# Kernel tuning notes

Measured on AMD Instinct MI355X. Metric: run time of the kernel, lower is better.

## Reference

```python
import jax, jax.numpy as jnp
import numpy as np

N = 16384   # must equal C**2 so the rel-pos embed broadcasts with x
C = 128     # in_channels
K = 9       # k (min legal for C=128: (2k-1)^2 >= 2C-1)
C_OUT = 256


def setup_inputs() -> dict:
    key = jax.random.key(0)
    k1, k2, k3 = jax.random.split(key, 3)
    x = jax.random.normal(k1, (N, C), dtype=jnp.float32)
    rel_pos_table = jax.random.normal(k2, ((2 * K - 1) ** 2, C), dtype=jnp.float32) * 0.02
    W = jax.random.normal(k3, (2 * C, C_OUT), dtype=jnp.float32) / np.float32(np.sqrt(2 * C))
    b = jnp.zeros((C_OUT,), dtype=jnp.float32)
    return {"x": x, "rel_pos_table": rel_pos_table, "W": W, "b": b}


def _knn_indices(x, k):
    # brute-force kNN (torch_cluster knn_graph, loop=False), dilation=1 -> no edge subsampling
    sq = jnp.sum(x * x, axis=-1)                       # [N]
    d = sq[:, None] + sq[None, :] - 2.0 * (x @ x.T)    # [N, N] squared distances
    d = d.at[jnp.diag_indices(x.shape[0])].set(jnp.inf)  # exclude self-loops
    _, idx = jax.lax.top_k(-d, k)                      # [N, k] nearest neighbors
    return idx


def reference(x, rel_pos_table, W, b):
    n, c = x.shape
    # 1) graph built on RAW x (before rel-pos add), as in the torch forward
    nbr = _knn_indices(x, K)                           # [N, K]
    # 2) learnable relative positional embedding: grid_size = x.shape[1] = C
    ar = jnp.arange(c)
    rel = (ar[:, None] - ar[None, :] + c - 1).reshape(-1)  # [C*C] == [N]
    x = x + rel_pos_table[rel]                         # [N, C]
    # 3) MRConv: max-relative aggregation + concat + 1x1 linear
    x_j = x[nbr]                                       # [N, K, C] neighbor gather
    m = jnp.max(x_j - x[:, None, :], axis=1)           # [N, C] max over neighbors
    return jnp.concatenate([x, m], axis=-1) @ W + b    # [N, C_OUT]
```

## Files before the change

kernel.cpp:

```cpp
#include <hip/hip_runtime.h>

#define NPTS 16384
#define CH 128
#define KNN 9
#define NCAND 12
#define NHALF 4
#define COUT 256
#define RG 8
#define RCAND 6

typedef __attribute__((ext_vector_type(8))) short bf16x8;
typedef __attribute__((ext_vector_type(4))) float f32x4;


__device__ __forceinline__ unsigned bfhi2(float x0, float x1) {
    unsigned u0 = __float_as_uint(x0), u1 = __float_as_uint(x1);
    unsigned r0 = (u0 + 0x7fffu + ((u0 >> 16) & 1u));
    unsigned r1 = (u1 + 0x7fffu + ((u1 >> 16) & 1u));
    return (r0 >> 16) | (r1 & 0xffff0000u);
}

struct TopL {
    float l0,l1,l2,l3,l4,l5,l6,l7,l8,l9,la,lb;
    int   m0,m1,m2,m3,m4,m5,m6,m7,m8,m9,ma,mb;
};
struct Top9 {
    float l0,l1,l2,l3,l4,l5,l6,l7,l8;
    int   m0,m1,m2,m3,m4,m5,m6,m7,m8;
};

__device__ __forceinline__ bool lexlt(float d, int g, float L, int M) {
    return d < L || (d == L && g < M);
}

__device__ __forceinline__ void ins12(TopL& T, float d, int g) {
    if (!lexlt(d, g, T.lb, T.mb)) return;
    bool b0 = lexlt(d,g,T.l0,T.m0);
    bool b1 = lexlt(d,g,T.l1,T.m1);
    bool b2 = lexlt(d,g,T.l2,T.m2);
    bool b3 = lexlt(d,g,T.l3,T.m3);
    bool b4 = lexlt(d,g,T.l4,T.m4);
    bool b5 = lexlt(d,g,T.l5,T.m5);
    bool b6 = lexlt(d,g,T.l6,T.m6);
    bool b7 = lexlt(d,g,T.l7,T.m7);
    bool b8 = lexlt(d,g,T.l8,T.m8);
    bool b9 = lexlt(d,g,T.l9,T.m9);
    bool ba = lexlt(d,g,T.la,T.ma);
    T.lb = ba ? T.la : d;               T.mb = ba ? T.ma : g;
    T.la = b9 ? T.l9 : (ba ? d : T.la); T.ma = b9 ? T.m9 : (ba ? g : T.ma);
    T.l9 = b8 ? T.l8 : (b9 ? d : T.l9); T.m9 = b8 ? T.m8 : (b9 ? g : T.m9);
    T.l8 = b7 ? T.l7 : (b8 ? d : T.l8); T.m8 = b7 ? T.m7 : (b8 ? g : T.m8);
    T.l7 = b6 ? T.l6 : (b7 ? d : T.l7); T.m7 = b6 ? T.m6 : (b7 ? g : T.m7);
    T.l6 = b5 ? T.l5 : (b6 ? d : T.l6); T.m6 = b5 ? T.m5 : (b6 ? g : T.m6);
    T.l5 = b4 ? T.l4 : (b5 ? d : T.l5); T.m5 = b4 ? T.m4 : (b5 ? g : T.m5);
    T.l4 = b3 ? T.l3 : (b4 ? d : T.l4); T.m4 = b3 ? T.m3 : (b4 ? g : T.m4);
    T.l3 = b2 ? T.l2 : (b3 ? d : T.l3); T.m3 = b2 ? T.m2 : (b3 ? g : T.m3);
    T.l2 = b1 ? T.l1 : (b2 ? d : T.l2); T.m2 = b1 ? T.m1 : (b2 ? g : T.m2);
    T.l1 = b0 ? T.l0 : (b1 ? d : T.l1); T.m1 = b0 ? T.m0 : (b1 ? g : T.m1);
    T.l0 = b0 ? d : T.l0;               T.m0 = b0 ? g : T.m0;
}

__device__ __forceinline__ void ins9(Top9& T, float d, int g) {
    if (!lexlt(d, g, T.l8, T.m8)) return;
    bool b0 = lexlt(d,g,T.l0,T.m0);
    bool b1 = lexlt(d,g,T.l1,T.m1);
    bool b2 = lexlt(d,g,T.l2,T.m2);
    bool b3 = lexlt(d,g,T.l3,T.m3);
    bool b4 = lexlt(d,g,T.l4,T.m4);
    bool b5 = lexlt(d,g,T.l5,T.m5);
    bool b6 = lexlt(d,g,T.l6,T.m6);
    bool b7 = lexlt(d,g,T.l7,T.m7);
    T.l8 = b7 ? T.l7 : d;               T.m8 = b7 ? T.m7 : g;
    T.l7 = b6 ? T.l6 : (b7 ? d : T.l7); T.m7 = b6 ? T.m6 : (b7 ? g : T.m7);
    T.l6 = b5 ? T.l5 : (b6 ? d : T.l6); T.m6 = b5 ? T.m5 : (b6 ? g : T.m6);
    T.l5 = b4 ? T.l4 : (b5 ? d : T.l5); T.m5 = b4 ? T.m4 : (b5 ? g : T.m5);
    T.l4 = b3 ? T.l3 : (b4 ? d : T.l4); T.m4 = b3 ? T.m3 : (b4 ? g : T.m4);
    T.l3 = b2 ? T.l2 : (b3 ? d : T.l3); T.m3 = b2 ? T.m2 : (b3 ? g : T.m3);
    T.l2 = b1 ? T.l1 : (b2 ? d : T.l2); T.m2 = b1 ? T.m1 : (b2 ? g : T.m2);
    T.l1 = b0 ? T.l0 : (b1 ? d : T.l1); T.m1 = b0 ? T.m0 : (b1 ? g : T.m1);
    T.l0 = b0 ? d : T.l0;               T.m0 = b0 ? g : T.m0;
}

__device__ __forceinline__ void merge_shfl(TopL& T, int mask) {
    TopL o;
    o.l0=__shfl_xor(T.l0,mask); o.m0=__shfl_xor(T.m0,mask);
    o.l1=__shfl_xor(T.l1,mask); o.m1=__shfl_xor(T.m1,mask);
    o.l2=__shfl_xor(T.l2,mask); o.m2=__shfl_xor(T.m2,mask);
    o.l3=__shfl_xor(T.l3,mask); o.m3=__shfl_xor(T.m3,mask);
    o.l4=__shfl_xor(T.l4,mask); o.m4=__shfl_xor(T.m4,mask);
    o.l5=__shfl_xor(T.l5,mask); o.m5=__shfl_xor(T.m5,mask);
    o.l6=__shfl_xor(T.l6,mask); o.m6=__shfl_xor(T.m6,mask);
    o.l7=__shfl_xor(T.l7,mask); o.m7=__shfl_xor(T.m7,mask);
    o.l8=__shfl_xor(T.l8,mask); o.m8=__shfl_xor(T.m8,mask);
    o.l9=__shfl_xor(T.l9,mask); o.m9=__shfl_xor(T.m9,mask);
    o.la=__shfl_xor(T.la,mask); o.ma=__shfl_xor(T.ma,mask);
    o.lb=__shfl_xor(T.lb,mask); o.mb=__shfl_xor(T.mb,mask);
    ins12(T,o.l0,o.m0); ins12(T,o.l1,o.m1); ins12(T,o.l2,o.m2);
    ins12(T,o.l3,o.m3); ins12(T,o.l4,o.m4); ins12(T,o.l5,o.m5);
    ins12(T,o.l6,o.m6); ins12(T,o.l7,o.m7); ins12(T,o.l8,o.m8);
    ins12(T,o.l9,o.m9); ins12(T,o.la,o.ma); ins12(T,o.lb,o.mb);
}

__device__ __forceinline__ void merge_shfl9(Top9& T, int mask) {
    Top9 o;
    o.l0=__shfl_xor(T.l0,mask); o.m0=__shfl_xor(T.m0,mask);
    o.l1=__shfl_xor(T.l1,mask); o.m1=__shfl_xor(T.m1,mask);
    o.l2=__shfl_xor(T.l2,mask); o.m2=__shfl_xor(T.m2,mask);
    o.l3=__shfl_xor(T.l3,mask); o.m3=__shfl_xor(T.m3,mask);
    o.l4=__shfl_xor(T.l4,mask); o.m4=__shfl_xor(T.m4,mask);
    o.l5=__shfl_xor(T.l5,mask); o.m5=__shfl_xor(T.m5,mask);
    o.l6=__shfl_xor(T.l6,mask); o.m6=__shfl_xor(T.m6,mask);
    o.l7=__shfl_xor(T.l7,mask); o.m7=__shfl_xor(T.m7,mask);
    o.l8=__shfl_xor(T.l8,mask); o.m8=__shfl_xor(T.m8,mask);
    ins9(T,o.l0,o.m0); ins9(T,o.l1,o.m1); ins9(T,o.l2,o.m2);
    ins9(T,o.l3,o.m3); ins9(T,o.l4,o.m4); ins9(T,o.l5,o.m5);
    ins9(T,o.l6,o.m6); ins9(T,o.l7,o.m7); ins9(T,o.l8,o.m8);
}

__global__ __launch_bounds__(256) void sqnp_kernel(const float* __restrict__ x,
                                                   float* __restrict__ sq) {
    const int i = blockIdx.x * 256 + threadIdx.x;
    const float4* row4 = (const float4*)(x + (size_t)i * CH);
    float r[8];
    {
        float4 a = row4[0], b = row4[1];
        r[0] = __fmul_rn(a.x, a.x); r[1] = __fmul_rn(a.y, a.y);
        r[2] = __fmul_rn(a.z, a.z); r[3] = __fmul_rn(a.w, a.w);
        r[4] = __fmul_rn(b.x, b.x); r[5] = __fmul_rn(b.y, b.y);
        r[6] = __fmul_rn(b.z, b.z); r[7] = __fmul_rn(b.w, b.w);
    }
#pragma unroll
    for (int g = 1; g < 16; ++g) {
        float4 a = row4[2 * g], b = row4[2 * g + 1];
        r[0] = __fadd_rn(r[0], __fmul_rn(a.x, a.x));
        r[1] = __fadd_rn(r[1], __fmul_rn(a.y, a.y));
        r[2] = __fadd_rn(r[2], __fmul_rn(a.z, a.z));
        r[3] = __fadd_rn(r[3], __fmul_rn(a.w, a.w));
        r[4] = __fadd_rn(r[4], __fmul_rn(b.x, b.x));
        r[5] = __fadd_rn(r[5], __fmul_rn(b.y, b.y));
        r[6] = __fadd_rn(r[6], __fmul_rn(b.z, b.z));
        r[7] = __fadd_rn(r[7], __fmul_rn(b.w, b.w));
    }
    float t0 = __fadd_rn(__fadd_rn(r[0], r[1]), __fadd_rn(r[2], r[3]));
    float t1 = __fadd_rn(__fadd_rn(r[4], r[5]), __fadd_rn(r[6], r[7]));
    sq[i] = __fadd_rn(t0, t1);
}

__global__ __launch_bounds__(256) void split_kernel(const float* __restrict__ x,
                                                    short* __restrict__ xhi) {
    const int P = blockIdx.x * 256 + threadIdx.x;
    const int r = P >> 4;
    const int s = P & 15;
    const int phys = s ^ (r & 15);
    const float4* src = (const float4*)(x + (size_t)r * CH) + s * 2;
    float4 f0 = src[0], f1 = src[1];
    uint4 h;
    h.x = bfhi2(f0.x, f0.y);
    h.y = bfhi2(f0.z, f0.w);
    h.z = bfhi2(f1.x, f1.y);
    h.w = bfhi2(f1.z, f1.w);
    *(uint4*)&xhi[(size_t)r * 128 + phys * 8] = h;
}

__global__ __launch_bounds__(256, 4) void knn_kernel(const short* __restrict__ xhi,
                                                     const float* __restrict__ sq,
                                                     unsigned short* __restrict__ cand) {
    __shared__ short Bhi[64 * 128];
    __shared__ float Dist[64 * 64];
    const int t = threadIdx.x;
    const int row0 = blockIdx.x * 64;
    const int half = blockIdx.y;
    const int ctbeg = half * (NPTS / NHALF);
    const int ctend = ctbeg + NPTS / NHALF;

    const int lane = t & 63;
    const int w = t >> 6;
    const int m = lane & 15;
    const int quad = lane >> 4;

#pragma unroll
    for (int it = 0; it < 4; ++it) {
        const int P = t + it * 256;
        *(uint4*)&Bhi[P * 8] = *(const uint4*)&xhi[(size_t)ctbeg * 128 + P * 8];
    }
    const short* arow = xhi + (size_t)(row0 + 16 * w + m) * 128;
    const bf16x8 a0 = *(const bf16x8*)&arow[((0 * 4 + quad) ^ m) * 8];
    const bf16x8 a1 = *(const bf16x8*)&arow[((1 * 4 + quad) ^ m) * 8];
    const bf16x8 a2 = *(const bf16x8*)&arow[((2 * 4 + quad) ^ m) * 8];
    const bf16x8 a3 = *(const bf16x8*)&arow[((3 * 4 + quad) ^ m) * 8];

    const float4 sqr4 = *(const float4*)&sq[row0 + 16 * w + quad * 4];

    TopL T;
    T.l0=T.l1=T.l2=T.l3=T.l4=T.l5=T.l6=T.l7=T.l8=T.l9=T.la=T.lb = __builtin_inff();
    T.m0=T.m1=T.m2=T.m3=T.m4=T.m5=T.m6=T.m7=T.m8=T.m9=T.ma=T.mb = 0x7fffffff;

    const int srow = t >> 2;
    const int sq4 = t & 3;
    const int srowg = row0 + srow;
    const float* drow = &Dist[srow * 64];
    const int sxor = srow & 63;

    for (int ct = ctbeg; ct < ctend; ct += 64) {
        __syncthreads();

        const float sqc0 = sq[ct + 0  + m];
        const float sqc1 = sq[ct + 16 + m];
        const float sqc2 = sq[ct + 32 + m];
        const float sqc3 = sq[ct + 48 + m];

        f32x4 acc0 = {0.f,0.f,0.f,0.f};
        f32x4 acc1 = {0.f,0.f,0.f,0.f};
        f32x4 acc2 = {0.f,0.f,0.f,0.f};
        f32x4 acc3 = {0.f,0.f,0.f,0.f};

#pragma unroll
        for (int kc = 0; kc < 4; ++kc) {
            const int ks = ((kc * 4 + quad) ^ m) * 8;
            const bf16x8 ah = (kc == 0) ? a0 : (kc == 1) ? a1 : (kc == 2) ? a2 : a3;
            bf16x8 bh0 = *(const bf16x8*)&Bhi[(0  + m) * 128 + ks];
            bf16x8 bh1 = *(const bf16x8*)&Bhi[(16 + m) * 128 + ks];
            bf16x8 bh2 = *(const bf16x8*)&Bhi[(32 + m) * 128 + ks];
            bf16x8 bh3 = *(const bf16x8*)&Bhi[(48 + m) * 128 + ks];
            acc0 = __builtin_amdgcn_mfma_f32_16x16x32_bf16(ah, bh0, acc0, 0, 0, 0);
            acc1 = __builtin_amdgcn_mfma_f32_16x16x32_bf16(ah, bh1, acc1, 0, 0, 0);
            acc2 = __builtin_amdgcn_mfma_f32_16x16x32_bf16(ah, bh2, acc2, 0, 0, 0);
            acc3 = __builtin_amdgcn_mfma_f32_16x16x32_bf16(ah, bh3, acc3, 0, 0, 0);
        }

#pragma unroll
        for (int reg = 0; reg < 4; ++reg) {
            const int row = 16 * w + quad * 4 + reg;
            const float sqr_r = (reg == 0) ? sqr4.x : (reg == 1) ? sqr4.y
                              : (reg == 2) ? sqr4.z : sqr4.w;
            const int c0 = 0  + m;
            const int c1 = 16 + m;
            const int c2 = 32 + m;
            const int c3 = 48 + m;
            Dist[row * 64 + (c0 ^ row)] = sqr_r + sqc0 - 2.f * acc0[reg];
            Dist[row * 64 + (c1 ^ row)] = sqr_r + sqc1 - 2.f * acc1[reg];
            Dist[row * 64 + (c2 ^ row)] = sqr_r + sqc2 - 2.f * acc2[reg];
            Dist[row * 64 + (c3 ^ row)] = sqr_r + sqc3 - 2.f * acc3[reg];
        }
        __syncthreads();

        const int ctn = ct + 64;
        uint4 pb0, pb1, pb2, pb3;
        if (ctn < ctend) {
            pb0 = *(const uint4*)&xhi[(size_t)ctn * 128 + (t +   0) * 8];
            pb1 = *(const uint4*)&xhi[(size_t)ctn * 128 + (t + 256) * 8];
            pb2 = *(const uint4*)&xhi[(size_t)ctn * 128 + (t + 512) * 8];
            pb3 = *(const uint4*)&xhi[(size_t)ctn * 128 + (t + 768) * 8];
        }

        float qd0 = __builtin_inff(), qd1 = __builtin_inff();
        int   qg0 = 0x7fffffff,      qg1 = 0x7fffffff;
        int   qn = 0;
#pragma unroll
        for (int k = 0; k < 16; ++k) {
            const int col = sq4 * 16 + k;
            const float d = drow[col ^ sxor];
            const int cg = ct + col;
            const bool pass = (cg != srowg) && lexlt(d, cg, T.lb, T.mb);
            if (pass) {
                if (qn >= 2) {
                    ins12(T, d, cg);
                } else if (qn == 0) {
                    qd0 = d; qg0 = cg;
                } else {
                    qd1 = d; qg1 = cg;
                }
                ++qn;
            }
        }
        if (qn > 0) ins12(T, qd0, qg0);
        if (qn > 1) ins12(T, qd1, qg1);

        if (ctn < ctend) {
            *(uint4*)&Bhi[(t +   0) * 8] = pb0;
            *(uint4*)&Bhi[(t + 256) * 8] = pb1;
            *(uint4*)&Bhi[(t + 512) * 8] = pb2;
            *(uint4*)&Bhi[(t + 768) * 8] = pb3;
        }
    }

    merge_shfl(T, 1);
    merge_shfl(T, 2);

    if (sq4 == 0) {
        unsigned short* cp_out = cand + (size_t)srowg * (NHALF * NCAND) + half * NCAND;
        cp_out[0]=(unsigned short)T.m0; cp_out[1]=(unsigned short)T.m1;
        cp_out[2]=(unsigned short)T.m2; cp_out[3]=(unsigned short)T.m3;
        cp_out[4]=(unsigned short)T.m4; cp_out[5]=(unsigned short)T.m5;
        cp_out[6]=(unsigned short)T.m6; cp_out[7]=(unsigned short)T.m7;
        cp_out[8]=(unsigned short)T.m8; cp_out[9]=(unsigned short)T.m9;
        cp_out[10]=(unsigned short)T.ma; cp_out[11]=(unsigned short)T.mb;
    }
}

__global__ __launch_bounds__(256) void refine_np_kernel(const float* __restrict__ x,
                                                        const float* __restrict__ sq,
                                                        const unsigned short* __restrict__ cand,
                                                        unsigned short* __restrict__ nbr) {
    const int gt = blockIdx.x * 256 + threadIdx.x;
    const int i = gt >> 3;
    const int g = gt & (RG - 1);
    const float4* X4 = (const float4*)x;
    const float sqi = sq[i];

    int ci[RCAND];
#pragma unroll
    for (int m = 0; m < RCAND; ++m)
        ci[m] = (int)cand[i * (NHALF * NCAND) + g * RCAND + m];
    float dot[RCAND];
#pragma unroll
    for (int m = 0; m < RCAND; ++m) dot[m] = 0.f;
#pragma unroll 4
    for (int c4 = 0; c4 < 32; ++c4) {
        float4 xv = X4[(size_t)i * 32 + c4];
#pragma unroll
        for (int m = 0; m < RCAND; ++m) {
            float4 nv = X4[(size_t)ci[m] * 32 + c4];
            float a = dot[m];
            a = __builtin_fmaf(xv.x, nv.x, a);
            a = __builtin_fmaf(xv.y, nv.y, a);
            a = __builtin_fmaf(xv.z, nv.z, a);
            a = __builtin_fmaf(xv.w, nv.w, a);
            dot[m] = a;
        }
    }

    Top9 T;
    T.l0=T.l1=T.l2=T.l3=T.l4=T.l5=T.l6=T.l7=T.l8 = __builtin_inff();
    T.m0=T.m1=T.m2=T.m3=T.m4=T.m5=T.m6=T.m7=T.m8 = 0x7fffffff;
#pragma unroll
    for (int m = 0; m < RCAND; ++m) {
        float s = __fadd_rn(sqi, sq[ci[m]]);
        float d = __fsub_rn(s, __fmul_rn(2.0f, dot[m]));
        ins9(T, d, ci[m]);
    }

    merge_shfl9(T, 1);
    merge_shfl9(T, 2);
    merge_shfl9(T, 4);

    if (g == 0) {
        unsigned short* np = nbr + (size_t)i * KNN;
        np[0]=(unsigned short)T.m0; np[1]=(unsigned short)T.m1; np[2]=(unsigned short)T.m2;
        np[3]=(unsigned short)T.m3; np[4]=(unsigned short)T.m4; np[5]=(unsigned short)T.m5;
        np[6]=(unsigned short)T.m6; np[7]=(unsigned short)T.m7; np[8]=(unsigned short)T.m8;
    }
}

__global__ __launch_bounds__(256, 2) void out_kernel(const float* __restrict__ x,
                                                     const float* __restrict__ tab,
                                                     const float* __restrict__ W,
                                                     const float* __restrict__ bias,
                                                     const unsigned short* __restrict__ nbr,
                                                     float* __restrict__ out) {
    __shared__ float cat[32][260];
    const int t = threadIdx.x;
    const int row0 = blockIdx.x * 32;
    {
        const int row = t >> 3;
        const int q = t & 7;
        const int i = row0 + row;
        const int rel_i = (i >> 7) - (i & 127) + 127;
        int nb[KNN], reln[KNN];
#pragma unroll
        for (int j = 0; j < KNN; ++j) {
            nb[j] = (int)nbr[i * KNN + j];
            reln[j] = (nb[j] >> 7) - (nb[j] & 127) + 127;
        }
        const float4* X4 = (const float4*)x;
        const float4* T4 = (const float4*)tab;
#pragma unroll
        for (int cc = 0; cc < 4; ++cc) {
            const int c4 = q * 4 + cc;
            float4 xv = X4[i * 32 + c4];
            float4 tv = T4[rel_i * 32 + c4];
            float4 xi;
            xi.x = xv.x + tv.x; xi.y = xv.y + tv.y; xi.z = xv.z + tv.z; xi.w = xv.w + tv.w;
            const float ninf = -__builtin_inff();
            float4 mx = {ninf, ninf, ninf, ninf};
#pragma unroll
            for (int j = 0; j < KNN; ++j) {
                float4 nv = X4[nb[j] * 32 + c4];
                float4 ntv = T4[reln[j] * 32 + c4];
                mx.x = fmaxf(mx.x, nv.x + ntv.x - xi.x);
                mx.y = fmaxf(mx.y, nv.y + ntv.y - xi.y);
                mx.z = fmaxf(mx.z, nv.z + ntv.z - xi.z);
                mx.w = fmaxf(mx.w, nv.w + ntv.w - xi.w);
            }
            *(float4*)&cat[row][c4 * 4] = xi;
            *(float4*)&cat[row][CH + c4 * 4] = mx;
        }
    }
    __syncthreads();

    float acc[32];
    const float bo = bias[t];
#pragma unroll
    for (int i = 0; i < 32; ++i) acc[i] = bo;
#pragma unroll 2
    for (int c0 = 0; c0 < 2 * CH; c0 += 4) {
        const float w0 = W[(c0 + 0) * COUT + t];
        const float w1 = W[(c0 + 1) * COUT + t];
        const float w2 = W[(c0 + 2) * COUT + t];
        const float w3 = W[(c0 + 3) * COUT + t];
#pragma unroll
        for (int i = 0; i < 32; ++i) {
            const float4 cv = *(const float4*)&cat[i][c0];
            acc[i] = fmaf(cv.x, w0, acc[i]);
            acc[i] = fmaf(cv.y, w1, acc[i]);
            acc[i] = fmaf(cv.z, w2, acc[i]);
            acc[i] = fmaf(cv.w, w3, acc[i]);
        }
    }
#pragma unroll
    for (int i = 0; i < 32; ++i) out[(size_t)(row0 + i) * COUT + t] = acc[i];
}

extern "C" void kernel_launch(void* const* d_in, const int* in_sizes, int n_in,
                              void* d_out, int out_size, void* d_ws, size_t ws_size,
                              hipStream_t stream) {
    (void)in_sizes; (void)n_in; (void)out_size; (void)ws_size;
    const float* x = (const float*)d_in[0];
    const float* tab = (const float*)d_in[1];
    const float* W = (const float*)d_in[2];
    const float* b = (const float*)d_in[3];
    float* out = (float*)d_out;

    char* ws = (char*)d_ws;
    float* sq = (float*)ws;
    unsigned short* nbr = (unsigned short*)(sq + NPTS);

    short* xhi = (short*)d_out;
    unsigned short* cand = (unsigned short*)((char*)d_out + ((size_t)NPTS * CH * 2));

    sqnp_kernel<<<NPTS / 256, 256, 0, stream>>>(x, sq);
    split_kernel<<<NPTS * 16 / 256, 256, 0, stream>>>(x, xhi);
    knn_kernel<<<dim3(NPTS / 64, NHALF), 256, 0, stream>>>(xhi, sq, cand);
    refine_np_kernel<<<NPTS * RG / 256, 256, 0, stream>>>(x, sq, cand, nbr);
    out_kernel<<<NPTS / 32, 256, 0, stream>>>(x, tab, W, b, nbr, out);
}
```

Measured before the change: 716.4 us.

## Split kNN candidate scan into eighths, drop row norm, specialize self-tile check

Splits the candidate-column range into 8 slices instead of 4, so the kNN kernel launches twice as many blocks. Each row now carries 96 candidates, and the refine kernel uses 16 threads per row with an extra shuffle merge step. The row's own squared norm is dropped from the distance, since it does not change the per-row ranking, which saves a load and an add. The self-loop check and lexicographic tie comparison are replaced by a plain <= test, with self-exclusion applied only on the tile that contains the diagonal. Occupancy is raised to 5 blocks per SIMD, which may increase register pressure, and the extra candidates add refine work.

```diff
diff --git a/kernel.cpp b/kernel.cpp
--- a/kernel.cpp
+++ b/kernel.cpp
@@ -4,9 +4,9 @@
 #define CH 128
 #define KNN 9
 #define NCAND 12
-#define NHALF 4
+#define NHALF 8
 #define COUT 256
-#define RG 8
+#define RG 16
 #define RCAND 6
 
 typedef __attribute__((ext_vector_type(8))) short bf16x8;
@@ -162,7 +162,7 @@
     *(uint4*)&xhi[(size_t)r * 128 + phys * 8] = h;
 }
 
-__global__ __launch_bounds__(256, 4) void knn_kernel(const short* __restrict__ xhi,
+__global__ __launch_bounds__(256, 5) void knn_kernel(const short* __restrict__ xhi,
                                                      const float* __restrict__ sq,
                                                      unsigned short* __restrict__ cand) {
     __shared__ short Bhi[64 * 128];
@@ -188,8 +188,6 @@
     const bf16x8 a1 = *(const bf16x8*)&arow[((1 * 4 + quad) ^ m) * 8];
     const bf16x8 a2 = *(const bf16x8*)&arow[((2 * 4 + quad) ^ m) * 8];
     const bf16x8 a3 = *(const bf16x8*)&arow[((3 * 4 + quad) ^ m) * 8];
-
-    const float4 sqr4 = *(const float4*)&sq[row0 + 16 * w + quad * 4];
 
     TopL T;
     T.l0=T.l1=T.l2=T.l3=T.l4=T.l5=T.l6=T.l7=T.l8=T.l9=T.la=T.lb = __builtin_inff();
@@ -231,16 +229,14 @@
 #pragma unroll
         for (int reg = 0; reg < 4; ++reg) {
             const int row = 16 * w + quad * 4 + reg;
-            const float sqr_r = (reg == 0) ? sqr4.x : (reg == 1) ? sqr4.y
-                              : (reg == 2) ? sqr4.z : sqr4.w;
             const int c0 = 0  + m;
             const int c1 = 16 + m;
             const int c2 = 32 + m;
             const int c3 = 48 + m;
-            Dist[row * 64 + (c0 ^ row)] = sqr_r + sqc0 - 2.f * acc0[reg];
-            Dist[row * 64 + (c1 ^ row)] = sqr_r + sqc1 - 2.f * acc1[reg];
-            Dist[row * 64 + (c2 ^ row)] = sqr_r + sqc2 - 2.f * acc2[reg];
-            Dist[row * 64 + (c3 ^ row)] = sqr_r + sqc3 - 2.f * acc3[reg];
+            Dist[row * 64 + (c0 ^ row)] = __builtin_fmaf(-2.f, acc0[reg], sqc0);
+            Dist[row * 64 + (c1 ^ row)] = __builtin_fmaf(-2.f, acc1[reg], sqc1);
+            Dist[row * 64 + (c2 ^ row)] = __builtin_fmaf(-2.f, acc2[reg], sqc2);
+            Dist[row * 64 + (c3 ^ row)] = __builtin_fmaf(-2.f, acc3[reg], sqc3);
         }
         __syncthreads();
 
@@ -256,21 +252,41 @@
         float qd0 = __builtin_inff(), qd1 = __builtin_inff();
         int   qg0 = 0x7fffffff,      qg1 = 0x7fffffff;
         int   qn = 0;
-#pragma unroll
-        for (int k = 0; k < 16; ++k) {
-            const int col = sq4 * 16 + k;
-            const float d = drow[col ^ sxor];
-            const int cg = ct + col;
-            const bool pass = (cg != srowg) && lexlt(d, cg, T.lb, T.mb);
-            if (pass) {
-                if (qn >= 2) {
-                    ins12(T, d, cg);
-                } else if (qn == 0) {
-                    qd0 = d; qg0 = cg;
-                } else {
-                    qd1 = d; qg1 = cg;
+        if (ct != row0) {
+#pragma unroll
+            for (int k = 0; k < 16; ++k) {
+                const int col = sq4 * 16 + k;
+                const float d = drow[col ^ sxor];
+                const bool pass = d <= T.lb;
+                if (pass) {
+                    const int cg = ct + col;
+                    if (qn >= 2) {
+                        ins12(T, d, cg);
+                    } else if (qn == 0) {
+                        qd0 = d; qg0 = cg;
+                    } else {
+                        qd1 = d; qg1 = cg;
+                    }
+                    ++qn;
                 }
-                ++qn;
+            }
+        } else {
+#pragma unroll
+            for (int k = 0; k < 16; ++k) {
+                const int col = sq4 * 16 + k;
+                const float d = drow[col ^ sxor];
+                const int cg = ct + col;
+                const bool pass = (cg != srowg) && (d <= T.lb);
+                if (pass) {
+                    if (qn >= 2) {
+                        ins12(T, d, cg);
+                    } else if (qn == 0) {
+                        qd0 = d; qg0 = cg;
+                    } else {
+                        qd1 = d; qg1 = cg;
+                    }
+                    ++qn;
+                }
             }
         }
         if (qn > 0) ins12(T, qd0, qg0);
@@ -303,7 +319,7 @@
                                                         const unsigned short* __restrict__ cand,
                                                         unsigned short* __restrict__ nbr) {
     const int gt = blockIdx.x * 256 + threadIdx.x;
-    const int i = gt >> 3;
+    const int i = gt >> 4;
     const int g = gt & (RG - 1);
     const float4* X4 = (const float4*)x;
     const float sqi = sq[i];
@@ -343,6 +359,7 @@
     merge_shfl9(T, 1);
     merge_shfl9(T, 2);
     merge_shfl9(T, 4);
+    merge_shfl9(T, 8);
 
     if (g == 0) {
         unsigned short* np = nbr + (size_t)i * KNN;
```

Result: slower. 1.834 ms (+156.0%).
